# Performance work log

Hardware: AMD Instinct MI355X
Metric: run time of the kernel (lower is better)

Reference implementation:

```python
import jax, jax.numpy as jnp
import numpy as np

B, D_IN, H = 32768, 256, 128
N_TASK, N_EXP, N_SHARE = 2, 4, 4


def setup_inputs() -> dict:
    key = jax.random.key(0)
    ks = jax.random.split(key, 4)
    s = 1.0 / np.sqrt(D_IN)
    return {
        "x": jax.random.normal(ks[0], (B, D_IN), dtype=jnp.float32),
        "W_share": jax.random.normal(ks[1], (N_SHARE, D_IN, H), dtype=jnp.float32) * s,
        "b_share": jnp.zeros((N_SHARE, H), dtype=jnp.float32),
        "W_task": jax.random.normal(ks[2], (N_TASK, N_EXP, D_IN, H), dtype=jnp.float32) * s,
        "b_task": jnp.zeros((N_TASK, N_EXP, H), dtype=jnp.float32),
        "W_gate": jax.random.normal(ks[3], (N_TASK, D_IN, N_SHARE + N_EXP), dtype=jnp.float32) * s,
        "b_gate": jnp.zeros((N_TASK, N_SHARE + N_EXP), dtype=jnp.float32),
    }


def reference(x, W_share, b_share, W_task, b_task, W_gate, b_gate):
    # shared experts: [B, N_SHARE, H]
    share = jax.nn.relu(jnp.einsum('bd,edh->beh', x, W_share) + b_share)
    # task-specific experts: [T, B, N_EXP, H]
    task = jax.nn.relu(jnp.einsum('bd,tedh->tbeh', x, W_task) + b_task[:, None])
    # gates: [T, B, N_SHARE + N_EXP], softmax over experts
    gate = jax.nn.softmax(jnp.einsum('bd,tdg->tbg', x, W_gate) + b_gate[:, None], axis=-1)
    # concat order matches original: share_net first, then task experts
    share_b = jnp.broadcast_to(share[None], (N_TASK, B, N_SHARE, H))
    experts = jnp.concatenate([share_b, task], axis=2)  # [T, B, N_SHARE+N_EXP, H]
    towers = jnp.einsum('tbeh,tbe->tbh', experts, gate)  # [T, B, H]
    return towers
```

## Files before the change

kernel.cpp:

```cpp
#include <hip/hip_runtime.h>


typedef __attribute__((ext_vector_type(8))) short short8;
typedef __attribute__((ext_vector_type(4))) float float4v;

#define ROW_US     136
#define ROW_B      272
#define UNIT_US    17408
#define UNIT_B     34816
#define WAVE_B     4352
#define WGT_OFF_US 417792
#define COPY_US    421888
#define COPY_B     843776

__device__ __forceinline__ unsigned short f2bf(float f) {
  unsigned u = __builtin_bit_cast(unsigned, f);
  u += 0x7FFFu + ((u >> 16) & 1u);
  return (unsigned short)(u >> 16);
}

__device__ __forceinline__ int slot2e(int sr, int t) {
  return (sr < 4) ? sr : 4 + t * 4 + (sr - 4);
}

__global__ __launch_bounds__(256)
void prep_kernel(const float* __restrict__ Ws,
                 const float* __restrict__ Wt,
                 const float* __restrict__ Wg,
                 unsigned short* __restrict__ WT, int NC) {
  int bid = blockIdx.x;
  int tid = threadIdx.x;
  if (bid < 96) {
    __shared__ float tile[64][65];
    int e  = bid >> 3;
    int kt = (bid >> 1) & 3;
    int ht = bid & 1;
    const float* src = (e < 4) ? Ws + ((size_t)e << 15)
                               : Wt + ((size_t)(e - 4) << 15);
    int m = tid & 15, n = tid >> 4;
    #pragma unroll
    for (int i = 0; i < 4; ++i) {
      int kl = i * 16 + n;
      float4 v = *(const float4*)&src[(size_t)(kt * 64 + kl) * 128 + ht * 64 + m * 4];
      tile[kl][m * 4 + 0] = v.x;
      tile[kl][m * 4 + 1] = v.y;
      tile[kl][m * 4 + 2] = v.z;
      tile[kl][m * 4 + 3] = v.w;
    }
    __syncthreads();
    #pragma unroll
    for (int i = 0; i < 4; ++i) {
      int hl = i * 16 + n;
      ushort4 o;
      o.x = f2bf(tile[m * 4 + 0][hl]);
      o.y = f2bf(tile[m * 4 + 1][hl]);
      o.z = f2bf(tile[m * 4 + 2][hl]);
      o.w = f2bf(tile[m * 4 + 3][hl]);
      size_t rowbase = (size_t)(e * 2 + (kt >> 1)) * UNIT_US
                     + (size_t)(ht * 64 + hl) * ROW_US + (kt & 1) * 64;
      for (int c = 0; c < NC; ++c) {
        *(ushort4*)&WT[(size_t)c * COPY_US + rowbase + m * 4] = o;
        if ((kt & 1) == 1 && m < 2) {
          ushort4 z = {0, 0, 0, 0};
          *(ushort4*)&WT[(size_t)c * COPY_US + rowbase + 64 + m * 4] = z;
        }
      }
    }
  } else {
    #pragma unroll
    for (int it = 0; it < 16; ++it) {
      int j = it * 256 + tid;
      int n = j >> 8, k = j & 255;
      int t = n >> 3, g = n & 7;
      unsigned short v = f2bf(Wg[(size_t)(t * 256 + k) * 8 + g]);
      for (int c = 0; c < NC; ++c)
        WT[(size_t)c * COPY_US + WGT_OFF_US + j] = v;
    }
  }
}

__global__ __launch_bounds__(512, 2)
void dmoe_main(const float* __restrict__ x,
               const unsigned short* __restrict__ WT,
               const float* __restrict__ b_share,
               const float* __restrict__ b_task,
               const float* __restrict__ b_gate,
               float* __restrict__ out, int NC) {
  __shared__ unsigned short Bs0[UNIT_US];
  __shared__ unsigned short Bs1[UNIT_US];
  __shared__ float gatesL[8 * 132];
  __shared__ float biasLds[8 * 128];

  const int tid  = threadIdx.x;
  const int lane = tid & 63;
  const int w    = tid >> 6;
  const int col  = lane & 15;
  const int quad = lane >> 4;
  const int mg   = w >> 1;
  const int ng   = w & 1;
  const int blk  = blockIdx.x;
  const int t    = blk & 1;
  const int rt   = blk >> 1;
  const int rot  = (blk >> 3) & 7;

  const char* WTc = (const char*)WT + (size_t)((blk >> 3) % NC) * COPY_B;

  const int e0 = slot2e(rot, t);
  uint4 p0, p1, p2, p3; unsigned p4;
  {
    const char* g = WTc + (size_t)(e0 * 2) * UNIT_B + w * WAVE_B;
    p0 = *(const uint4*)(g + lane * 16);
    p1 = *(const uint4*)(g + 1024 + lane * 16);
    p2 = *(const uint4*)(g + 2048 + lane * 16);
    p3 = *(const uint4*)(g + 3072 + lane * 16);
    p4 = *(const unsigned*)(g + 4096 + lane * 4);
  }

  short8 A[2][8];
  {
    const float* xb = x + ((size_t)rt * 128 + mg * 32 + col) * 256 + quad * 8;
    #pragma unroll
    for (int mt = 0; mt < 2; ++mt) {
      const float* xr = xb + (size_t)mt * 16 * 256;
      #pragma unroll
      for (int k = 0; k < 8; ++k) {
        float4v u = __builtin_nontemporal_load((const float4v*)(xr + k * 32));
        float4v v = __builtin_nontemporal_load((const float4v*)(xr + k * 32 + 4));
        short8 fr;
        fr[0] = (short)f2bf(u[0]); fr[1] = (short)f2bf(u[1]);
        fr[2] = (short)f2bf(u[2]); fr[3] = (short)f2bf(u[3]);
        fr[4] = (short)f2bf(v[0]); fr[5] = (short)f2bf(v[1]);
        fr[6] = (short)f2bf(v[2]); fr[7] = (short)f2bf(v[3]);
        A[mt][k] = fr;
      }
    }
  }

  for (int i = tid; i < 1024; i += 512) {
    int sr = i >> 7, h = i & 127;
    biasLds[i] = (sr < 4) ? b_share[sr * 128 + h]
                          : b_task[(size_t)(t * 4 + (sr - 4)) * 128 + h];
  }

  {
    const unsigned short* WgT = (const unsigned short*)(WTc + WGT_OFF_US * 2);
    const int gr = col & 7;
    const unsigned short* bp = WgT + (size_t)(t * 8 + gr) * 256 + quad * 8;
    short8 Bg[8];
    #pragma unroll
    for (int k = 0; k < 8; ++k) Bg[k] = *(const short8*)(bp + k * 32);
    float bg = b_gate[t * 8 + gr];
    #pragma unroll
    for (int mt = 0; mt < 2; ++mt) {
      float4v ag = {0.f, 0.f, 0.f, 0.f};
      #pragma unroll
      for (int k = 0; k < 8; ++k)
        ag = __builtin_amdgcn_mfma_f32_16x16x32_bf16(A[mt][k], Bg[k], ag, 0, 0, 0);
      #pragma unroll
      for (int r = 0; r < 4; ++r) {
        float vlog = ag[r] + bg;
        float m = vlog;
        m = fmaxf(m, __shfl_xor(m, 1));
        m = fmaxf(m, __shfl_xor(m, 2));
        m = fmaxf(m, __shfl_xor(m, 4));
        float p = __expf(vlog - m);
        float s = p;
        s += __shfl_xor(s, 1);
        s += __shfl_xor(s, 2);
        s += __shfl_xor(s, 4);
        if (ng == 0 && col < 8)
          gatesL[col * 132 + mg * 32 + mt * 16 + quad * 4 + r] = p / s;
      }
    }
  }

  {
    char* l = (char*)Bs0 + w * WAVE_B;
    *(uint4*)(l + lane * 16)        = p0;
    *(uint4*)(l + 1024 + lane * 16) = p1;
    *(uint4*)(l + 2048 + lane * 16) = p2;
    *(uint4*)(l + 3072 + lane * 16) = p3;
    *(unsigned*)(l + 4096 + lane * 4) = p4;
  }
  __syncthreads();

  float tw[2][4][4];
  #pragma unroll
  for (int mt = 0; mt < 2; ++mt)
    #pragma unroll
    for (int nt = 0; nt < 4; ++nt)
      #pragma unroll
      for (int r = 0; r < 4; ++r)
        tw[mt][nt][r] = 0.f;

  const int hb = ng * 64;
  float4v acc[2][4];

  #pragma unroll 1
  for (int s = 0; s < 8; ++s) {
    const int sr  = (s + rot) & 7;
    const int e   = slot2e(sr, t);
    const int sr2 = (s + 1 + rot) & 7;
    const int e2  = slot2e(sr2, t);
    #pragma unroll
    for (int kh = 0; kh < 2; ++kh) {
      uint4 q0, q1, q2, q3; unsigned q4;
      const bool doStage = !(s == 7 && kh == 1);
      if (doStage) {
        const int un = (kh == 0) ? (e * 2 + 1) : (e2 * 2);
        const char* g = WTc + (size_t)un * UNIT_B + w * WAVE_B;
        q0 = *(const uint4*)(g + lane * 16);
        q1 = *(const uint4*)(g + 1024 + lane * 16);
        q2 = *(const uint4*)(g + 2048 + lane * 16);
        q3 = *(const uint4*)(g + 3072 + lane * 16);
        q4 = *(const unsigned*)(g + 4096 + lane * 4);
      }
      if (kh == 0) {
        #pragma unroll
        for (int mt = 0; mt < 2; ++mt)
          #pragma unroll
          for (int nt = 0; nt < 4; ++nt)
            acc[mt][nt] = (float4v){0.f, 0.f, 0.f, 0.f};
      }
      {
        const char* Bb = (const char*)(kh ? Bs1 : Bs0);
        #pragma unroll
        for (int kk = 0; kk < 4; ++kk) {
          #pragma unroll
          for (int nt = 0; nt < 4; ++nt) {
            short8 bfr = *(const short8*)(Bb + (hb + nt * 16 + col) * ROW_B
                                          + kk * 64 + quad * 16);
            acc[0][nt] = __builtin_amdgcn_mfma_f32_16x16x32_bf16(
                A[0][kh * 4 + kk], bfr, acc[0][nt], 0, 0, 0);
            acc[1][nt] = __builtin_amdgcn_mfma_f32_16x16x32_bf16(
                A[1][kh * 4 + kk], bfr, acc[1][nt], 0, 0, 0);
          }
        }
      }
      if (doStage) {
        char* l = (char*)(kh ? Bs0 : Bs1) + w * WAVE_B;
        *(uint4*)(l + lane * 16)        = q0;
        *(uint4*)(l + 1024 + lane * 16) = q1;
        *(uint4*)(l + 2048 + lane * 16) = q2;
        *(uint4*)(l + 3072 + lane * 16) = q3;
        *(unsigned*)(l + 4096 + lane * 4) = q4;
      }
      if (kh == 1) {
        #pragma unroll
        for (int mt = 0; mt < 2; ++mt) {
          int rb = mg * 32 + mt * 16 + quad * 4;
          float4 g = *(const float4*)&gatesL[sr * 132 + rb];
          #pragma unroll
          for (int nt = 0; nt < 4; ++nt) {
            float bias = biasLds[sr * 128 + hb + nt * 16 + col];
            #pragma unroll
            for (int r = 0; r < 4; ++r) {
              float v = fmaxf(acc[mt][nt][r] + bias, 0.f);
              tw[mt][nt][r] += ((const float*)&g)[r] * v;
            }
          }
        }
      }
      __syncthreads();
    }
  }

  #pragma unroll
  for (int mt = 0; mt < 2; ++mt)
    #pragma unroll
    for (int r = 0; r < 4; ++r) {
      size_t row = (size_t)rt * 128 + mg * 32 + mt * 16 + quad * 4 + r;
      float* op = out + ((size_t)t << 22) + row * 128 + hb;
      #pragma unroll
      for (int nt = 0; nt < 4; ++nt)
        __builtin_nontemporal_store(tw[mt][nt][r], op + nt * 16 + col);
    }
}

extern "C" void kernel_launch(void* const* d_in, const int* in_sizes, int n_in,
                              void* d_out, int out_size, void* d_ws, size_t ws_size,
                              hipStream_t stream) {
  const float* x       = (const float*)d_in[0];
  const float* W_share = (const float*)d_in[1];
  const float* b_share = (const float*)d_in[2];
  const float* W_task  = (const float*)d_in[3];
  const float* b_task  = (const float*)d_in[4];
  const float* W_gate  = (const float*)d_in[5];
  const float* b_gate  = (const float*)d_in[6];
  float* out = (float*)d_out;
  unsigned short* WT = (unsigned short*)d_ws;

  int NC = (int)(ws_size / (size_t)COPY_B);
  if (NC < 1) NC = 1;
  if (NC > 2) NC = 2;

  prep_kernel<<<97, 256, 0, stream>>>(W_share, W_task, W_gate, WT, NC);
  dmoe_main<<<512, 512, 0, stream>>>(x, WT, b_share, b_task, b_gate, out, NC);
}
```

Before: 156.6 us.

## Stage expert weights via direct global-to-LDS loads with triple buffering

Replaces the register-staged weight copies into LDS with global_load_lds direct transfers and moves from double to triple buffering of weight units. Synchronisation now uses explicit vmcnt waits and raw barriers. The wave layout changes from 4x2 to 2x4, so each wave computes 64 rows by 32 columns and holds more A fragments. MFMA sections are wrapped in setprio. The goal is to remove the VGPR round-trip and the full syncthreads stalls when staging weights. In exchange it uses more LDS and registers and drops occupancy to one block per CU. The hand-written vmcnt counts are fragile.

```diff
diff --git a/kernel.cpp b/kernel.cpp
--- a/kernel.cpp
+++ b/kernel.cpp
@@ -21,6 +21,15 @@
 
 __device__ __forceinline__ int slot2e(int sr, int t) {
   return (sr < 4) ? sr : 4 + t * 4 + (sr - 4);
+}
+
+typedef const __attribute__((address_space(1))) unsigned int GBUF;
+typedef __attribute__((address_space(3))) unsigned int LBUF;
+__device__ __forceinline__ void gll16(const void* g, void* l) {
+  __builtin_amdgcn_global_load_lds((GBUF*)g, (LBUF*)l, 16, 0, 0);
+}
+__device__ __forceinline__ void gll4(const void* g, void* l) {
+  __builtin_amdgcn_global_load_lds((GBUF*)g, (LBUF*)l, 4, 0, 0);
 }
 
 __global__ __launch_bounds__(256)
@@ -79,7 +88,7 @@
   }
 }
 
-__global__ __launch_bounds__(512, 2)
+__global__ __launch_bounds__(512, 1)
 void dmoe_main(const float* __restrict__ x,
                const unsigned short* __restrict__ WT,
                const float* __restrict__ b_share,
@@ -88,6 +97,7 @@
                float* __restrict__ out, int NC) {
   __shared__ unsigned short Bs0[UNIT_US];
   __shared__ unsigned short Bs1[UNIT_US];
+  __shared__ unsigned short Bs2[UNIT_US];
   __shared__ float gatesL[8 * 132];
   __shared__ float biasLds[8 * 128];
 
@@ -96,8 +106,8 @@
   const int w    = tid >> 6;
   const int col  = lane & 15;
   const int quad = lane >> 4;
-  const int mg   = w >> 1;
-  const int ng   = w & 1;
+  const int mg   = w >> 2;
+  const int ng   = w & 3;
   const int blk  = blockIdx.x;
   const int t    = blk & 1;
   const int rt   = blk >> 1;
@@ -105,22 +115,25 @@
 
   const char* WTc = (const char*)WT + (size_t)((blk >> 3) % NC) * COPY_B;
 
+  auto stage = [&](int un, unsigned short* dst) {
+    const char* g = WTc + (size_t)un * UNIT_B + w * WAVE_B;
+    char* l = (char*)dst + w * WAVE_B;
+    gll16(g + lane * 16,        l);
+    gll16(g + 1024 + lane * 16, l + 1024);
+    gll16(g + 2048 + lane * 16, l + 2048);
+    gll16(g + 3072 + lane * 16, l + 3072);
+    gll4 (g + 4096 + lane * 4,  l + 4096);
+  };
+
   const int e0 = slot2e(rot, t);
-  uint4 p0, p1, p2, p3; unsigned p4;
+  stage(e0 * 2,     Bs0);
+  stage(e0 * 2 + 1, Bs1);
+
+  short8 A[4][8];
   {
-    const char* g = WTc + (size_t)(e0 * 2) * UNIT_B + w * WAVE_B;
-    p0 = *(const uint4*)(g + lane * 16);
-    p1 = *(const uint4*)(g + 1024 + lane * 16);
-    p2 = *(const uint4*)(g + 2048 + lane * 16);
-    p3 = *(const uint4*)(g + 3072 + lane * 16);
-    p4 = *(const unsigned*)(g + 4096 + lane * 4);
-  }
-
-  short8 A[2][8];
-  {
-    const float* xb = x + ((size_t)rt * 128 + mg * 32 + col) * 256 + quad * 8;
-    #pragma unroll
-    for (int mt = 0; mt < 2; ++mt) {
+    const float* xb = x + ((size_t)rt * 128 + mg * 64 + col) * 256 + quad * 8;
+    #pragma unroll
+    for (int mt = 0; mt < 4; ++mt) {
       const float* xr = xb + (size_t)mt * 16 * 256;
       #pragma unroll
       for (int k = 0; k < 8; ++k) {
@@ -151,7 +164,7 @@
     for (int k = 0; k < 8; ++k) Bg[k] = *(const short8*)(bp + k * 32);
     float bg = b_gate[t * 8 + gr];
     #pragma unroll
-    for (int mt = 0; mt < 2; ++mt) {
+    for (int mt = 0; mt < 4; ++mt) {
       float4v ag = {0.f, 0.f, 0.f, 0.f};
       #pragma unroll
       for (int k = 0; k < 8; ++k)
@@ -169,110 +182,112 @@
         s += __shfl_xor(s, 2);
         s += __shfl_xor(s, 4);
         if (ng == 0 && col < 8)
-          gatesL[col * 132 + mg * 32 + mt * 16 + quad * 4 + r] = p / s;
-      }
-    }
-  }
-
-  {
-    char* l = (char*)Bs0 + w * WAVE_B;
-    *(uint4*)(l + lane * 16)        = p0;
-    *(uint4*)(l + 1024 + lane * 16) = p1;
-    *(uint4*)(l + 2048 + lane * 16) = p2;
-    *(uint4*)(l + 3072 + lane * 16) = p3;
-    *(unsigned*)(l + 4096 + lane * 4) = p4;
-  }
-  __syncthreads();
-
-  float tw[2][4][4];
+          gatesL[col * 132 + mg * 64 + mt * 16 + quad * 4 + r] = p / s;
+      }
+    }
+  }
+
+  asm volatile("s_waitcnt lgkmcnt(0)" ::: "memory");
+
+  float tw[4][2][4];
   #pragma unroll
-  for (int mt = 0; mt < 2; ++mt)
-    #pragma unroll
-    for (int nt = 0; nt < 4; ++nt)
+  for (int mt = 0; mt < 4; ++mt)
+    #pragma unroll
+    for (int nt = 0; nt < 2; ++nt)
       #pragma unroll
       for (int r = 0; r < 4; ++r)
         tw[mt][nt][r] = 0.f;
 
-  const int hb = ng * 64;
-  float4v acc[2][4];
+  const int hb = ng * 32;
+  const int lrow = (hb + col) * ROW_B + quad * 16;
+  float4v acc[4][2];
+
+  unsigned short* bA = Bs0;
+  unsigned short* bB = Bs1;
+  unsigned short* bC = Bs2;
 
   #pragma unroll 1
   for (int s = 0; s < 8; ++s) {
-    const int sr  = (s + rot) & 7;
-    const int e   = slot2e(sr, t);
-    const int sr2 = (s + 1 + rot) & 7;
-    const int e2  = slot2e(sr2, t);
-    #pragma unroll
-    for (int kh = 0; kh < 2; ++kh) {
-      uint4 q0, q1, q2, q3; unsigned q4;
-      const bool doStage = !(s == 7 && kh == 1);
-      if (doStage) {
-        const int un = (kh == 0) ? (e * 2 + 1) : (e2 * 2);
-        const char* g = WTc + (size_t)un * UNIT_B + w * WAVE_B;
-        q0 = *(const uint4*)(g + lane * 16);
-        q1 = *(const uint4*)(g + 1024 + lane * 16);
-        q2 = *(const uint4*)(g + 2048 + lane * 16);
-        q3 = *(const uint4*)(g + 3072 + lane * 16);
-        q4 = *(const unsigned*)(g + 4096 + lane * 4);
-      }
-      if (kh == 0) {
+    const int sr = (s + rot) & 7;
+    const int en = slot2e((s + 1 + rot) & 7, t);
+
+    asm volatile("s_waitcnt vmcnt(5)" ::: "memory");
+    __builtin_amdgcn_s_barrier();
+    asm volatile("" ::: "memory");
+    if (s < 7) stage(en * 2, bC);
+    asm volatile("" ::: "memory");
+    #pragma unroll
+    for (int mt = 0; mt < 4; ++mt)
+      #pragma unroll
+      for (int nt = 0; nt < 2; ++nt)
+        acc[mt][nt] = (float4v){0.f, 0.f, 0.f, 0.f};
+    {
+      const char* L = (const char*)bA + lrow;
+      __builtin_amdgcn_s_setprio(1);
+      #pragma unroll
+      for (int kk = 0; kk < 4; ++kk) {
         #pragma unroll
-        for (int mt = 0; mt < 2; ++mt)
+        for (int nt = 0; nt < 2; ++nt) {
+          short8 bfr = *(const short8*)(L + nt * (16 * ROW_B) + kk * 64);
           #pragma unroll
-          for (int nt = 0; nt < 4; ++nt)
-            acc[mt][nt] = (float4v){0.f, 0.f, 0.f, 0.f};
-      }
-      {
-        const char* Bb = (const char*)(kh ? Bs1 : Bs0);
+          for (int mt = 0; mt < 4; ++mt)
+            acc[mt][nt] = __builtin_amdgcn_mfma_f32_16x16x32_bf16(
+                A[mt][kk], bfr, acc[mt][nt], 0, 0, 0);
+        }
+      }
+      __builtin_amdgcn_s_setprio(0);
+    }
+
+    if (s < 7) asm volatile("s_waitcnt vmcnt(5)" ::: "memory");
+    else       asm volatile("s_waitcnt vmcnt(0)" ::: "memory");
+    __builtin_amdgcn_s_barrier();
+    asm volatile("" ::: "memory");
+    if (s < 7) stage(en * 2 + 1, bA);
+    asm volatile("" ::: "memory");
+    {
+      const char* L = (const char*)bB + lrow;
+      __builtin_amdgcn_s_setprio(1);
+      #pragma unroll
+      for (int kk = 0; kk < 4; ++kk) {
         #pragma unroll
-        for (int kk = 0; kk < 4; ++kk) {
+        for (int nt = 0; nt < 2; ++nt) {
+          short8 bfr = *(const short8*)(L + nt * (16 * ROW_B) + kk * 64);
           #pragma unroll
-          for (int nt = 0; nt < 4; ++nt) {
-            short8 bfr = *(const short8*)(Bb + (hb + nt * 16 + col) * ROW_B
-                                          + kk * 64 + quad * 16);
-            acc[0][nt] = __builtin_amdgcn_mfma_f32_16x16x32_bf16(
-                A[0][kh * 4 + kk], bfr, acc[0][nt], 0, 0, 0);
-            acc[1][nt] = __builtin_amdgcn_mfma_f32_16x16x32_bf16(
-                A[1][kh * 4 + kk], bfr, acc[1][nt], 0, 0, 0);
-          }
+          for (int mt = 0; mt < 4; ++mt)
+            acc[mt][nt] = __builtin_amdgcn_mfma_f32_16x16x32_bf16(
+                A[mt][4 + kk], bfr, acc[mt][nt], 0, 0, 0);
         }
       }
-      if (doStage) {
-        char* l = (char*)(kh ? Bs0 : Bs1) + w * WAVE_B;
-        *(uint4*)(l + lane * 16)        = q0;
-        *(uint4*)(l + 1024 + lane * 16) = q1;
-        *(uint4*)(l + 2048 + lane * 16) = q2;
-        *(uint4*)(l + 3072 + lane * 16) = q3;
-        *(unsigned*)(l + 4096 + lane * 4) = q4;
-      }
-      if (kh == 1) {
+      __builtin_amdgcn_s_setprio(0);
+    }
+
+    #pragma unroll
+    for (int mt = 0; mt < 4; ++mt) {
+      int rb = mg * 64 + mt * 16 + quad * 4;
+      float4 g = *(const float4*)&gatesL[sr * 132 + rb];
+      #pragma unroll
+      for (int nt = 0; nt < 2; ++nt) {
+        float bias = biasLds[sr * 128 + hb + nt * 16 + col];
         #pragma unroll
-        for (int mt = 0; mt < 2; ++mt) {
-          int rb = mg * 32 + mt * 16 + quad * 4;
-          float4 g = *(const float4*)&gatesL[sr * 132 + rb];
-          #pragma unroll
-          for (int nt = 0; nt < 4; ++nt) {
-            float bias = biasLds[sr * 128 + hb + nt * 16 + col];
-            #pragma unroll
-            for (int r = 0; r < 4; ++r) {
-              float v = fmaxf(acc[mt][nt][r] + bias, 0.f);
-              tw[mt][nt][r] += ((const float*)&g)[r] * v;
-            }
-          }
+        for (int r = 0; r < 4; ++r) {
+          float v = fmaxf(acc[mt][nt][r] + bias, 0.f);
+          tw[mt][nt][r] += ((const float*)&g)[r] * v;
         }
       }
-      __syncthreads();
-    }
+    }
+
+    unsigned short* tmp = bA;
+    bA = bC; bC = bB; bB = tmp;
   }
 
   #pragma unroll
-  for (int mt = 0; mt < 2; ++mt)
+  for (int mt = 0; mt < 4; ++mt)
     #pragma unroll
     for (int r = 0; r < 4; ++r) {
-      size_t row = (size_t)rt * 128 + mg * 32 + mt * 16 + quad * 4 + r;
+      size_t row = (size_t)rt * 128 + mg * 64 + mt * 16 + quad * 4 + r;
       float* op = out + ((size_t)t << 22) + row * 128 + hb;
       #pragma unroll
-      for (int nt = 0; nt < 4; ++nt)
+      for (int nt = 0; nt < 2; ++nt)
         __builtin_nontemporal_store(tw[mt][nt][r], op + nt * 16 + col);
     }
 }
```

Measured after the change: 213.2 us. 36.1% more time.

## Split H dimension across blocks with 256-thread blocks and 64-row tiles

Applied to the files above, without the earlier changes.

Each block now handles 64 rows and one 64-wide half of H, using 256 threads and a grid of 2048 blocks instead of 512. The goal is finer-grained parallelism and higher occupancy from smaller LDS staging buffers, with launch bounds set to 4 blocks per CU. The change also raises MFMA issue priority around the inner GEMM, interleaves the gate MFMAs across both M tiles, and drops the nontemporal hint on x loads. In exchange, x is loaded and converted to bf16 twice per row, and the gate softmax is recomputed by both H-half blocks.

```diff
diff --git a/kernel.cpp b/kernel.cpp
--- a/kernel.cpp
+++ b/kernel.cpp
@@ -8,6 +8,7 @@
 #define ROW_B      272
 #define UNIT_US    17408
 #define UNIT_B     34816
+#define HUNIT_B    17408
 #define WAVE_B     4352
 #define WGT_OFF_US 417792
 #define COPY_US    421888
@@ -79,17 +80,17 @@
   }
 }
 
-__global__ __launch_bounds__(512, 2)
+__global__ __launch_bounds__(256, 4)
 void dmoe_main(const float* __restrict__ x,
                const unsigned short* __restrict__ WT,
                const float* __restrict__ b_share,
                const float* __restrict__ b_task,
                const float* __restrict__ b_gate,
                float* __restrict__ out, int NC) {
-  __shared__ unsigned short Bs0[UNIT_US];
-  __shared__ unsigned short Bs1[UNIT_US];
-  __shared__ float gatesL[8 * 132];
-  __shared__ float biasLds[8 * 128];
+  __shared__ unsigned short Bs0[HUNIT_B / 2];
+  __shared__ unsigned short Bs1[HUNIT_B / 2];
+  __shared__ float gatesL[8 * 68];
+  __shared__ float biasLds[8 * 64];
 
   const int tid  = threadIdx.x;
   const int lane = tid & 63;
@@ -100,32 +101,43 @@
   const int ng   = w & 1;
   const int blk  = blockIdx.x;
   const int t    = blk & 1;
-  const int rt   = blk >> 1;
+  const int hh   = (blk >> 1) & 1;
+  const int rt   = blk >> 2;
   const int rot  = (blk >> 3) & 7;
 
   const char* WTc = (const char*)WT + (size_t)((blk >> 3) % NC) * COPY_B;
 
-  const int e0 = slot2e(rot, t);
   uint4 p0, p1, p2, p3; unsigned p4;
-  {
-    const char* g = WTc + (size_t)(e0 * 2) * UNIT_B + w * WAVE_B;
+  auto stageIssue = [&](int un) {
+    const char* g = WTc + (size_t)un * UNIT_B + hh * HUNIT_B + w * WAVE_B;
     p0 = *(const uint4*)(g + lane * 16);
     p1 = *(const uint4*)(g + 1024 + lane * 16);
     p2 = *(const uint4*)(g + 2048 + lane * 16);
     p3 = *(const uint4*)(g + 3072 + lane * 16);
     p4 = *(const unsigned*)(g + 4096 + lane * 4);
-  }
+  };
+  auto deposit = [&](unsigned short* dst) {
+    char* l = (char*)dst + w * WAVE_B;
+    *(uint4*)(l + lane * 16)        = p0;
+    *(uint4*)(l + 1024 + lane * 16) = p1;
+    *(uint4*)(l + 2048 + lane * 16) = p2;
+    *(uint4*)(l + 3072 + lane * 16) = p3;
+    *(unsigned*)(l + 4096 + lane * 4) = p4;
+  };
+
+  const int e0 = slot2e(rot, t);
+  stageIssue(e0 * 2);
 
   short8 A[2][8];
   {
-    const float* xb = x + ((size_t)rt * 128 + mg * 32 + col) * 256 + quad * 8;
+    const float* xb = x + ((size_t)rt * 64 + mg * 32 + col) * 256 + quad * 8;
     #pragma unroll
     for (int mt = 0; mt < 2; ++mt) {
       const float* xr = xb + (size_t)mt * 16 * 256;
       #pragma unroll
       for (int k = 0; k < 8; ++k) {
-        float4v u = __builtin_nontemporal_load((const float4v*)(xr + k * 32));
-        float4v v = __builtin_nontemporal_load((const float4v*)(xr + k * 32 + 4));
+        float4v u = *(const float4v*)(xr + k * 32);
+        float4v v = *(const float4v*)(xr + k * 32 + 4);
         short8 fr;
         fr[0] = (short)f2bf(u[0]); fr[1] = (short)f2bf(u[1]);
         fr[2] = (short)f2bf(u[2]); fr[3] = (short)f2bf(u[3]);
@@ -136,8 +148,10 @@
     }
   }
 
-  for (int i = tid; i < 1024; i += 512) {
-    int sr = i >> 7, h = i & 127;
+  deposit(Bs0);
+
+  for (int i = tid; i < 512; i += 256) {
+    int sr = i >> 6, hl = i & 63, h = hh * 64 + hl;
     biasLds[i] = (sr < 4) ? b_share[sr * 128 + h]
                           : b_task[(size_t)(t * 4 + (sr - 4)) * 128 + h];
   }
@@ -146,19 +160,24 @@
     const unsigned short* WgT = (const unsigned short*)(WTc + WGT_OFF_US * 2);
     const int gr = col & 7;
     const unsigned short* bp = WgT + (size_t)(t * 8 + gr) * 256 + quad * 8;
-    short8 Bg[8];
-    #pragma unroll
-    for (int k = 0; k < 8; ++k) Bg[k] = *(const short8*)(bp + k * 32);
     float bg = b_gate[t * 8 + gr];
+    float4v ag[2] = {{0.f,0.f,0.f,0.f},{0.f,0.f,0.f,0.f}};
+    #pragma unroll
+    for (int kb = 0; kb < 2; ++kb) {
+      short8 Bg[4];
+      #pragma unroll
+      for (int j = 0; j < 4; ++j) Bg[j] = *(const short8*)(bp + (kb * 4 + j) * 32);
+      #pragma unroll
+      for (int j = 0; j < 4; ++j) {
+        ag[0] = __builtin_amdgcn_mfma_f32_16x16x32_bf16(A[0][kb * 4 + j], Bg[j], ag[0], 0, 0, 0);
+        ag[1] = __builtin_amdgcn_mfma_f32_16x16x32_bf16(A[1][kb * 4 + j], Bg[j], ag[1], 0, 0, 0);
+      }
+    }
     #pragma unroll
     for (int mt = 0; mt < 2; ++mt) {
-      float4v ag = {0.f, 0.f, 0.f, 0.f};
-      #pragma unroll
-      for (int k = 0; k < 8; ++k)
-        ag = __builtin_amdgcn_mfma_f32_16x16x32_bf16(A[mt][k], Bg[k], ag, 0, 0, 0);
       #pragma unroll
       for (int r = 0; r < 4; ++r) {
-        float vlog = ag[r] + bg;
+        float vlog = ag[mt][r] + bg;
         float m = vlog;
         m = fmaxf(m, __shfl_xor(m, 1));
         m = fmaxf(m, __shfl_xor(m, 2));
@@ -169,65 +188,47 @@
         s += __shfl_xor(s, 2);
         s += __shfl_xor(s, 4);
         if (ng == 0 && col < 8)
-          gatesL[col * 132 + mg * 32 + mt * 16 + quad * 4 + r] = p / s;
-      }
-    }
-  }
-
-  {
-    char* l = (char*)Bs0 + w * WAVE_B;
-    *(uint4*)(l + lane * 16)        = p0;
-    *(uint4*)(l + 1024 + lane * 16) = p1;
-    *(uint4*)(l + 2048 + lane * 16) = p2;
-    *(uint4*)(l + 3072 + lane * 16) = p3;
-    *(unsigned*)(l + 4096 + lane * 4) = p4;
+          gatesL[col * 68 + mg * 32 + mt * 16 + quad * 4 + r] = p / s;
+      }
+    }
   }
   __syncthreads();
 
-  float tw[2][4][4];
+  float tw[2][2][4];
   #pragma unroll
   for (int mt = 0; mt < 2; ++mt)
     #pragma unroll
-    for (int nt = 0; nt < 4; ++nt)
+    for (int nt = 0; nt < 2; ++nt)
       #pragma unroll
       for (int r = 0; r < 4; ++r)
         tw[mt][nt][r] = 0.f;
 
-  const int hb = ng * 64;
-  float4v acc[2][4];
+  const int hb = ng * 32;
+  float4v acc[2][2];
 
   #pragma unroll 1
   for (int s = 0; s < 8; ++s) {
     const int sr  = (s + rot) & 7;
     const int e   = slot2e(sr, t);
-    const int sr2 = (s + 1 + rot) & 7;
-    const int e2  = slot2e(sr2, t);
+    const int e2  = slot2e((s + 1 + rot) & 7, t);
     #pragma unroll
     for (int kh = 0; kh < 2; ++kh) {
-      uint4 q0, q1, q2, q3; unsigned q4;
       const bool doStage = !(s == 7 && kh == 1);
-      if (doStage) {
-        const int un = (kh == 0) ? (e * 2 + 1) : (e2 * 2);
-        const char* g = WTc + (size_t)un * UNIT_B + w * WAVE_B;
-        q0 = *(const uint4*)(g + lane * 16);
-        q1 = *(const uint4*)(g + 1024 + lane * 16);
-        q2 = *(const uint4*)(g + 2048 + lane * 16);
-        q3 = *(const uint4*)(g + 3072 + lane * 16);
-        q4 = *(const unsigned*)(g + 4096 + lane * 4);
-      }
+      if (doStage) stageIssue(kh == 0 ? e * 2 + 1 : e2 * 2);
       if (kh == 0) {
         #pragma unroll
         for (int mt = 0; mt < 2; ++mt)
           #pragma unroll
-          for (int nt = 0; nt < 4; ++nt)
+          for (int nt = 0; nt < 2; ++nt)
             acc[mt][nt] = (float4v){0.f, 0.f, 0.f, 0.f};
       }
       {
         const char* Bb = (const char*)(kh ? Bs1 : Bs0);
+        __builtin_amdgcn_s_setprio(1);
         #pragma unroll
         for (int kk = 0; kk < 4; ++kk) {
           #pragma unroll
-          for (int nt = 0; nt < 4; ++nt) {
+          for (int nt = 0; nt < 2; ++nt) {
             short8 bfr = *(const short8*)(Bb + (hb + nt * 16 + col) * ROW_B
                                           + kk * 64 + quad * 16);
             acc[0][nt] = __builtin_amdgcn_mfma_f32_16x16x32_bf16(
@@ -236,23 +237,17 @@
                 A[1][kh * 4 + kk], bfr, acc[1][nt], 0, 0, 0);
           }
         }
-      }
-      if (doStage) {
-        char* l = (char*)(kh ? Bs0 : Bs1) + w * WAVE_B;
-        *(uint4*)(l + lane * 16)        = q0;
-        *(uint4*)(l + 1024 + lane * 16) = q1;
-        *(uint4*)(l + 2048 + lane * 16) = q2;
-        *(uint4*)(l + 3072 + lane * 16) = q3;
-        *(unsigned*)(l + 4096 + lane * 4) = q4;
-      }
+        __builtin_amdgcn_s_setprio(0);
+      }
+      if (doStage) deposit(kh ? Bs0 : Bs1);
       if (kh == 1) {
         #pragma unroll
         for (int mt = 0; mt < 2; ++mt) {
           int rb = mg * 32 + mt * 16 + quad * 4;
-          float4 g = *(const float4*)&gatesL[sr * 132 + rb];
+          float4 g = *(const float4*)&gatesL[sr * 68 + rb];
           #pragma unroll
-          for (int nt = 0; nt < 4; ++nt) {
-            float bias = biasLds[sr * 128 + hb + nt * 16 + col];
+          for (int nt = 0; nt < 2; ++nt) {
+            float bias = biasLds[sr * 64 + hb + nt * 16 + col];
             #pragma unroll
             for (int r = 0; r < 4; ++r) {
               float v = fmaxf(acc[mt][nt][r] + bias, 0.f);
@@ -269,10 +264,10 @@
   for (int mt = 0; mt < 2; ++mt)
     #pragma unroll
     for (int r = 0; r < 4; ++r) {
-      size_t row = (size_t)rt * 128 + mg * 32 + mt * 16 + quad * 4 + r;
-      float* op = out + ((size_t)t << 22) + row * 128 + hb;
-      #pragma unroll
-      for (int nt = 0; nt < 4; ++nt)
+      size_t row = (size_t)rt * 64 + mg * 32 + mt * 16 + quad * 4 + r;
+      float* op = out + ((size_t)t << 22) + row * 128 + hh * 64 + hb;
+      #pragma unroll
+      for (int nt = 0; nt < 2; ++nt)
         __builtin_nontemporal_store(tw[mt][nt][r], op + nt * 16 + col);
     }
 }
@@ -295,5 +290,5 @@
   if (NC > 2) NC = 2;
 
   prep_kernel<<<97, 256, 0, stream>>>(W_share, W_task, W_gate, WT, NC);
-  dmoe_main<<<512, 512, 0, stream>>>(x, WT, b_share, b_task, b_gate, out, NC);
-}
+  dmoe_main<<<2048, 256, 0, stream>>>(x, WT, b_share, b_task, b_gate, out, NC);
+}
```

New measurement: 213.2 us. 36.1% more time.
